# Performance work log

Measured on AMD Instinct MI355X. Metric: run time of the kernel, lower is better.

The kernel has to match this reference:

```python
import jax, jax.numpy as jnp
import numpy as np

B = 4; C = 3; IMG = 256; P = 16; HP = 16; HW = 256
DIM = 512; DEPTH = 6; HEADS = 8; DH = 64
NS = 50; SH = 4; SDH = 64; ITERS = 3; RPD = 128; FF = 2048; N = NS + HW


def _ln(x, g, b):
    m = jnp.mean(x, -1, keepdims=True)
    v = jnp.var(x, -1, keepdims=True)
    return (x - m) * jax.lax.rsqrt(v + 1e-5) * g + b


def _rms(x, g):
    # lucidrains RMSNorm: F.normalize(x, dim=-1) * sqrt(dim) * gamma
    n = jnp.linalg.norm(x, axis=-1, keepdims=True)
    return x / jnp.maximum(n, 1e-12) * (DIM ** 0.5) * g


def setup_inputs() -> dict:
    key = jax.random.key(0)
    ks = iter(jax.random.split(key, 64))
    def W(*s):
        return jax.random.normal(next(ks), s, jnp.float32) * 0.02
    SI = SH * SDH
    d = {}
    d['images'] = jax.random.normal(next(ks), (B, C, IMG, IMG), jnp.float32)
    d['slot_noise'] = jax.random.normal(next(ks), (B, NS, DIM), jnp.float32)
    d['patch_w'] = W(C * P * P, DIM); d['patch_b'] = jnp.zeros((DIM,))
    d['hpos'] = W(HP, DIM); d['wpos'] = W(HP, DIM)
    d['rp_w1'] = W(2, RPD); d['rp_b1'] = jnp.zeros((RPD,))
    d['rp_w2'] = W(RPD, RPD); d['rp_b2'] = jnp.zeros((RPD,))
    d['rp_w3'] = W(RPD, HEADS); d['rp_b3'] = jnp.zeros((HEADS,))
    d['slots_mu'] = W(1, 1, DIM); d['slots_logsigma'] = jnp.zeros((1, 1, DIM))
    d['sa_ln_in_g'] = jnp.ones((DIM,)); d['sa_ln_in_b'] = jnp.zeros((DIM,))
    d['sa_ln_sl_g'] = jnp.ones((DIM,)); d['sa_ln_sl_b'] = jnp.zeros((DIM,))
    d['sa_wq'] = W(DIM, SI); d['sa_bq'] = jnp.zeros((SI,))
    d['sa_wk'] = W(DIM, SI); d['sa_bk'] = jnp.zeros((SI,))
    d['sa_wv'] = W(DIM, SI); d['sa_bv'] = jnp.zeros((SI,))
    d['sa_wo'] = W(SI, DIM); d['sa_bo'] = jnp.zeros((DIM,))
    d['gru_wih'] = W(DIM, 3 * DIM); d['gru_whh'] = W(DIM, 3 * DIM)
    d['gru_bih'] = jnp.zeros((3 * DIM,)); d['gru_bhh'] = jnp.zeros((3 * DIM,))
    d['sa_ln_ff_g'] = jnp.ones((DIM,)); d['sa_ln_ff_b'] = jnp.zeros((DIM,))
    d['sa_mlp_w1'] = W(DIM, DIM); d['sa_mlp_b1'] = jnp.zeros((DIM,))
    d['sa_mlp_w2'] = W(DIM, DIM); d['sa_mlp_b2'] = jnp.zeros((DIM,))
    d['s2c_w'] = W(DIM, 2); d['s2c_b'] = jnp.zeros((2,))
    d['attn_g'] = jnp.ones((DEPTH, DIM))
    d['wq'] = W(DEPTH, DIM, HEADS * DH); d['wk'] = W(DEPTH, DIM, HEADS * DH)
    d['wv'] = W(DEPTH, DIM, HEADS * DH); d['wo'] = W(DEPTH, HEADS * DH, DIM)
    d['ff_g'] = jnp.ones((DEPTH, DIM))
    d['ff_w1'] = W(DEPTH, DIM, FF); d['ff_b1'] = jnp.zeros((DEPTH, FF))
    d['ff_w2'] = W(DEPTH, FF, DIM); d['ff_b2'] = jnp.zeros((DEPTH, DIM))
    d['final_g'] = jnp.ones((DIM,))
    d['pred_w'] = W(DIM, DIM); d['pred_b'] = jnp.zeros((DIM,))
    return d


def reference(images, slot_noise, patch_w, patch_b, hpos, wpos,
              rp_w1, rp_b1, rp_w2, rp_b2, rp_w3, rp_b3,
              slots_mu, slots_logsigma, sa_ln_in_g, sa_ln_in_b, sa_ln_sl_g, sa_ln_sl_b,
              sa_wq, sa_bq, sa_wk, sa_bk, sa_wv, sa_bv, sa_wo, sa_bo,
              gru_wih, gru_whh, gru_bih, gru_bhh, sa_ln_ff_g, sa_ln_ff_b,
              sa_mlp_w1, sa_mlp_b1, sa_mlp_w2, sa_mlp_b2, s2c_w, s2c_b,
              attn_g, wq, wk, wv, wo, ff_g, ff_w1, ff_b1, ff_w2, ff_b2,
              final_g, pred_w, pred_b):
    b = images.shape[0]
    # patchify: b c (h p1) (w p2) -> b h w (p1 p2 c)
    x = images.reshape(b, C, HP, P, HP, P).transpose(0, 2, 4, 3, 5, 1).reshape(b, HP, HP, P * P * C)
    tokens = x @ patch_w + patch_b                     # [b, HP, HP, DIM]
    tokens = tokens + hpos[:, None, :] + wpos[None, :, :]
    tokens = tokens.reshape(b, HW, DIM)
    # --- multi-head slot attention ---
    inp = _ln(tokens, sa_ln_in_g, sa_ln_in_b)
    k = (inp @ sa_wk + sa_bk).reshape(b, HW, SH, SDH).transpose(0, 2, 1, 3)
    v = (inp @ sa_wv + sa_bv).reshape(b, HW, SH, SDH).transpose(0, 2, 1, 3)
    slots = slots_mu + jnp.exp(slots_logsigma) * slot_noise  # [b, NS, DIM]
    scale = SDH ** -0.5
    for _ in range(ITERS):
        prev = slots
        s = _ln(slots, sa_ln_sl_g, sa_ln_sl_b)
        q = (s @ sa_wq + sa_bq).reshape(b, NS, SH, SDH).transpose(0, 2, 1, 3)
        dots = jnp.einsum('bhid,bhjd->bhij', q, k) * scale     # [b, SH, NS, HW]
        attn = jax.nn.softmax(dots, axis=-2) + 1e-8            # softmax over slots
        attn = attn / jnp.sum(attn, -1, keepdims=True)         # weighted mean over inputs
        upd = jnp.einsum('bhij,bhjd->bhid', attn, v)
        upd = upd.transpose(0, 2, 1, 3).reshape(b, NS, SH * SDH) @ sa_wo + sa_bo
        # GRUCell(updates, prev_slots)
        gx = upd @ gru_wih + gru_bih
        gh = prev @ gru_whh + gru_bhh
        xr, xz, xn = jnp.split(gx, 3, -1)
        hr, hz, hn = jnp.split(gh, 3, -1)
        r = jax.nn.sigmoid(xr + hr)
        z = jax.nn.sigmoid(xz + hz)
        nn_ = jnp.tanh(xn + r * hn)
        slots = (1 - z) * nn_ + z * prev
        slots = slots + (jax.nn.relu(_ln(slots, sa_ln_ff_g, sa_ln_ff_b) @ sa_mlp_w1 + sa_mlp_b1) @ sa_mlp_w2 + sa_mlp_b2)
    objects = slots
    slot_coords = objects @ s2c_w + s2c_b              # [b, NS, 2]
    # --- relative position MLP bias (slots coords + patch grid) ---
    g = jnp.arange(HP, dtype=jnp.float32)
    grid = jnp.stack(jnp.meshgrid(g, g, indexing='ij'), -1).reshape(HW, 2)
    coords = jnp.concatenate([slot_coords, jnp.broadcast_to(grid, (b, HW, 2))], axis=1)  # [b, N, 2]
    rel = coords[:, :, None, :] - coords[:, None, :, :]   # [b, N, N, 2]
    hmid = jax.nn.silu(rel @ rp_w1 + rp_b1)
    hmid = jax.nn.silu(hmid @ rp_w2 + rp_b2)
    bias = jnp.transpose(hmid @ rp_w3 + rp_b3, (0, 3, 1, 2))  # [b, HEADS, N, N]
    # --- transformer with per-layer rel-pos bias ---
    x = jnp.concatenate([objects, tokens], axis=1)     # [b, N, DIM]
    ascale = DH ** -0.5
    for l in range(DEPTH):
        h = _rms(x, attn_g[l])
        qh = (h @ wq[l]).reshape(b, N, HEADS, DH).transpose(0, 2, 1, 3)
        kh = (h @ wk[l]).reshape(b, N, HEADS, DH).transpose(0, 2, 1, 3)
        vh = (h @ wv[l]).reshape(b, N, HEADS, DH).transpose(0, 2, 1, 3)
        sim = jnp.einsum('bhid,bhjd->bhij', qh, kh) * ascale + bias
        a = jax.nn.softmax(sim, -1)
        o = jnp.einsum('bhij,bhjd->bhid', a, vh).transpose(0, 2, 1, 3).reshape(b, N, HEADS * DH) @ wo[l]
        x = x + o
        h = _rms(x, ff_g[l])
        x = x + (jax.nn.gelu(h @ ff_w1[l] + ff_b1[l]) @ ff_w2[l] + ff_b2[l])
    x = _rms(x, final_g)
    return x[:, NS:] @ pred_w + pred_b                 # [b, HW, DIM]
```

## Files before the change

### kernel.cpp

```cpp
#include <hip/hip_runtime.h>
#include <hip/hip_bf16.h>

typedef __hip_bfloat16 bf16;
typedef short short8v __attribute__((ext_vector_type(8)));
typedef float float4v __attribute__((ext_vector_type(4)));

static __device__ __forceinline__ float b2f(bf16 x){ return __bfloat162float(x); }

static __device__ __forceinline__ float ldin(const void* p, size_t i, bool isbf) {
  return isbf ? b2f(((const bf16*)p)[i]) : ((const float*)p)[i];
}

static __device__ __forceinline__ unsigned short f2bu(float f) {
  bf16 h = __float2bfloat16(f);
  return *reinterpret_cast<unsigned short*>(&h);
}

#define CDIV(a,b) (((a)+(b)-1)/(b))

#define NB   4
#define NSL  50
#define HWT  256
#define NT   306
#define DIM  512
#define NH   8
#define FF   2048
#define RPP  28100
#define PCH  56200

static __device__ __forceinline__ void rp_decode(int q, int& i, int& j) {
  if (q < 15300) { i = q / NT; j = q % NT; }
  else { int r = q - 15300; i = NSL + r / NSL; j = r % NSL; }
}

__global__ void detect_k(const void* p, int* flag) {
  const unsigned short* u = (const unsigned short*)p;
  int t = threadIdx.x;
  int e = (u[t] >> 7) & 0xFF;
  __shared__ int anybad;
  if (t == 0) anybad = 0;
  __syncthreads();
  if (e >= 0x88) atomicOr(&anybad, 1);
  __syncthreads();
  if (t == 0) *flag = anybad ? 0 : 1;
}

struct WtArgs {
  const void* W[17];
  unsigned long long wto[17];
  int K[17], N[17];
  int base[18];
};

__global__ __launch_bounds__(256) void wtrans_all_k(WtArgs a, unsigned short* __restrict__ WT,
                                                    const int* __restrict__ flagp) {
  const bool isbf = *flagp != 0;
  int bid = blockIdx.x;
  int idx = 0;
#pragma unroll
  for (int i = 1; i < 17; ++i) if (bid >= a.base[i]) idx = i;
  int t0 = bid - a.base[idx];
  const int K = a.K[idx], N = a.N[idx];
  const int tilesN = N >> 6;
  const int perLayer = tilesN * (K >> 6);
  const int layer = t0 / perLayer, rem = t0 % perLayer;
  const int n0 = (rem % tilesN) * 64, k0 = (rem / tilesN) * 64;
  const void* W = a.W[idx];
  unsigned short* dst0 = WT + a.wto[idx];
  const size_t slice = (size_t)K * N * layer;

  __shared__ unsigned short S[64 * 72];
  int t = threadIdx.x;
  int kk = t >> 4, nn = (t & 15) * 4;
#pragma unroll
  for (int r = 0; r < 4; ++r) {
    int k = k0 + kk + r * 16;
    unsigned short v[4];
    if (isbf) {
      ushort4 u = *(const ushort4*)((const unsigned short*)W + slice + (size_t)k * N + n0 + nn);
      v[0]=u.x; v[1]=u.y; v[2]=u.z; v[3]=u.w;
    } else {
      float4 f = *(const float4*)((const float*)W + slice + (size_t)k * N + n0 + nn);
      v[0]=f2bu(f.x); v[1]=f2bu(f.y); v[2]=f2bu(f.z); v[3]=f2bu(f.w);
    }
#pragma unroll
    for (int i = 0; i < 4; ++i) S[(nn + i) * 72 + kk + r * 16] = v[i];
  }
  __syncthreads();
  int nr = t >> 2, kc = (t & 3) * 16;
  short8v s0 = *(const short8v*)&S[nr * 72 + kc];
  short8v s1 = *(const short8v*)&S[nr * 72 + kc + 8];
  unsigned short* dst = dst0 + slice + (size_t)(n0 + nr) * K + k0 + kc;
  *(short8v*)dst = s0;
  *(short8v*)(dst + 8) = s1;
}

#define LDK 72
static __device__ __forceinline__ void gemm_body2(
    const void* __restrict__ A, int aty,
    const unsigned short* __restrict__ WT,
    const void* __restrict__ bias, size_t boff,
    void* __restrict__ C, int oty,
    int M, int N, int K, int kbeg, int kend,
    int act, int mode, int spec,
    const void* __restrict__ p0, const void* __restrict__ p1,
    bool isbf)
{
  __shared__ unsigned short As[64 * LDK];
  __shared__ unsigned short Bs[64 * LDK];
  const int tid = threadIdx.x;
  const int lane = tid & 63, wave = tid >> 6;
  const int quad = lane >> 4, ti = lane & 15;
  const int wm = (wave & 1) * 32, wn = (wave >> 1) * 32;
  const int bm = blockIdx.y * 64, bn = blockIdx.x * 64;
  const int srow = tid >> 2, sch = (tid & 3) * 16;

  unsigned short ha[16], hb[16];
  const int gm = bm + srow;
  const bool aok = gm < M;
  const unsigned short* Abf = (const unsigned short*)A + (size_t)gm * K;
  const float*          Af  = (const float*)A + (size_t)gm * K;
  const unsigned short* Bp  = WT + (size_t)(bn + srow) * K;

  auto fetchA = [&](int k0) {
    if (aok) {
      if (aty) {
        const ushort4* ap = (const ushort4*)(Abf + k0 + sch);
#pragma unroll
        for (int i = 0; i < 4; ++i) {
          ushort4 u = ap[i];
          ha[i*4+0]=u.x; ha[i*4+1]=u.y; ha[i*4+2]=u.z; ha[i*4+3]=u.w;
        }
      } else {
        const float4* ap = (const float4*)(Af + k0 + sch);
#pragma unroll
        for (int i = 0; i < 4; ++i) {
          float4 f = ap[i];
          ha[i*4+0]=f2bu(f.x); ha[i*4+1]=f2bu(f.y); ha[i*4+2]=f2bu(f.z); ha[i*4+3]=f2bu(f.w);
        }
      }
    } else {
#pragma unroll
      for (int i = 0; i < 16; ++i) ha[i] = 0;
    }
  };
  auto fetchB = [&](int k0) {
    const ushort4* bp = (const ushort4*)(Bp + k0 + sch);
#pragma unroll
    for (int i = 0; i < 4; ++i) {
      ushort4 u = bp[i];
      hb[i*4+0]=u.x; hb[i*4+1]=u.y; hb[i*4+2]=u.z; hb[i*4+3]=u.w;
    }
  };

  float4v acc00 = {0,0,0,0}, acc01 = {0,0,0,0}, acc10 = {0,0,0,0}, acc11 = {0,0,0,0};
  fetchA(kbeg); fetchB(kbeg);
  for (int k0 = kbeg; k0 < kend; k0 += 64) {
    *(short8v*)&As[srow * LDK + sch]     = *(short8v*)ha;
    *(short8v*)&As[srow * LDK + sch + 8] = *(short8v*)(ha + 8);
    *(short8v*)&Bs[srow * LDK + sch]     = *(short8v*)hb;
    *(short8v*)&Bs[srow * LDK + sch + 8] = *(short8v*)(hb + 8);
    __syncthreads();
    if (k0 + 64 < kend) { fetchA(k0 + 64); fetchB(k0 + 64); }
#pragma unroll
    for (int ks = 0; ks < 2; ++ks) {
      short8v a0 = *reinterpret_cast<const short8v*>(&As[(wm + ti)      * LDK + ks * 32 + quad * 8]);
      short8v a1 = *reinterpret_cast<const short8v*>(&As[(wm + 16 + ti) * LDK + ks * 32 + quad * 8]);
      short8v b0 = *reinterpret_cast<const short8v*>(&Bs[(wn + ti)      * LDK + ks * 32 + quad * 8]);
      short8v b1 = *reinterpret_cast<const short8v*>(&Bs[(wn + 16 + ti) * LDK + ks * 32 + quad * 8]);
      acc00 = __builtin_amdgcn_mfma_f32_16x16x32_bf16(a0, b0, acc00, 0, 0, 0);
      acc01 = __builtin_amdgcn_mfma_f32_16x16x32_bf16(a0, b1, acc01, 0, 0, 0);
      acc10 = __builtin_amdgcn_mfma_f32_16x16x32_bf16(a1, b0, acc10, 0, 0, 0);
      acc11 = __builtin_amdgcn_mfma_f32_16x16x32_bf16(a1, b1, acc11, 0, 0, 0);
    }
    __syncthreads();
  }

  float4v accs[2][2] = {{acc00, acc01}, {acc10, acc11}};
#pragma unroll
  for (int mi = 0; mi < 2; ++mi) {
#pragma unroll
    for (int ni = 0; ni < 2; ++ni) {
      int row0 = bm + wm + mi * 16 + quad * 4;
      int col  = bn + wn + ni * 16 + ti;
      float bv = (bias && kbeg == 0) ? ldin(bias, boff + col, isbf) : 0.f;
#pragma unroll
      for (int r = 0; r < 4; ++r) {
        int row = row0 + r;
        if (row >= M) continue;
        float v = accs[mi][ni][r] + bv;
        if (act == 1) v = fmaxf(v, 0.f);
        else if (act == 2) {
          float u = 0.7978845608028654f * (v + 0.044715f * v * v * v);
          v = 0.5f * v * (1.f + tanhf(u));
        } else if (act == 3) {
          v = v / (1.f + expf(-v));
        }
        if (spec == 2 && kbeg == 0) {
          int hh = (row >> 4) & 15, ww = row & 15;
          v += ldin(p0, hh * N + col, isbf) + ldin(p1, ww * N + col, isbf);
        }
        if (spec == 1) {
          int b_ = row / NT, n_ = row % NT;
          if (n_ >= NSL) {
            size_t oi = ((size_t)(b_ * HWT + (n_ - NSL))) * N + col;
            if (isbf) ((bf16*)C)[oi] = __float2bfloat16(v);
            else      ((float*)C)[oi] = v;
          }
        } else {
          size_t idx = (size_t)row * N + col;
          if (oty) ((bf16*)C)[idx] = __float2bfloat16(v);
          else {
            float* Cf = (float*)C;
            if (mode == 2) atomicAdd(&Cf[idx], v);
            else if (mode == 1) Cf[idx] += v;
            else Cf[idx] = v;
          }
        }
      }
    }
  }
}

__global__ __launch_bounds__(256) void gemm_mfma(
    const void* A, int aty, const unsigned short* WT, size_t woff,
    const void* bias, size_t boff, void* C, int oty,
    int M, int N, int K, int act, int accum, int zsplit,
    int spec, const void* p0, const void* p1, const int* __restrict__ flagp)
{
  int ksz = K / zsplit;
  int kbeg = blockIdx.z * ksz;
  int mode = zsplit > 1 ? 2 : (accum ? 1 : 0);
  gemm_body2(A, aty, WT + woff, bias, boff, C, oty, M, N, K, kbeg, kbeg + ksz,
             act, mode, spec, p0, p1, *flagp != 0);
}

__global__ __launch_bounds__(256) void gemm_mfma_tri(
    const void* A, int aty, const unsigned short* WT, size_t o0, size_t o1, size_t o2,
    void* C0, void* C1, void* C2, int oty, int M, int N, int K,
    const int* __restrict__ flagp)
{
  size_t o = blockIdx.z == 0 ? o0 : (blockIdx.z == 1 ? o1 : o2);
  void* C = blockIdx.z == 0 ? C0 : (blockIdx.z == 1 ? C1 : C2);
  gemm_body2(A, aty, WT + o, nullptr, 0, C, oty, M, N, K, 0, K, 0, 0, 0,
             nullptr, nullptr, *flagp != 0);
}

__global__ __launch_bounds__(256) void gemm_mfma_duo(
    const void* A0, const void* A1, int aty, const unsigned short* WT, size_t o0, size_t o1,
    const void* bias0, const void* bias1, void* C0, void* C1, int oty,
    int M, int N, int K, const int* __restrict__ flagp)
{
  const void* A = blockIdx.z ? A1 : A0;
  size_t o = blockIdx.z ? o1 : o0;
  const void* bias = blockIdx.z ? bias1 : bias0;
  void* C = blockIdx.z ? C1 : C0;
  gemm_body2(A, aty, WT + o, bias, 0, C, oty, M, N, K, 0, K, 0, 0, 0,
             nullptr, nullptr, *flagp != 0);
}

__global__ void coords_k(const float* __restrict__ slots, const void* __restrict__ w,
                         const void* __restrict__ bv, float* __restrict__ coords,
                         const int* __restrict__ flagp) {
  const bool isbf = *flagp != 0;
  __shared__ float r0[256], r1[256];
  int blk = blockIdx.x, t = threadIdx.x;
  if (blk < 200) {
    int b = blk / 50, n = blk % 50;
    const float* x = slots + (size_t)blk * DIM;
    float v0 = x[t], v1 = x[t + 256];
    float a0 = v0 * ldin(w, 2 * t, isbf)     + v1 * ldin(w, 2 * (t + 256), isbf);
    float a1 = v0 * ldin(w, 2 * t + 1, isbf) + v1 * ldin(w, 2 * (t + 256) + 1, isbf);
    r0[t] = a0; r1[t] = a1;
    __syncthreads();
    for (int o = 128; o > 0; o >>= 1) {
      if (t < o) { r0[t] += r0[t + o]; r1[t] += r1[t + o]; }
      __syncthreads();
    }
    if (t == 0) {
      coords[((size_t)b * NT + n) * 2]     = r0[0] + ldin(bv, 0, isbf);
      coords[((size_t)b * NT + n) * 2 + 1] = r1[0] + ldin(bv, 1, isbf);
    }
  } else {
#pragma unroll
    for (int s = 0; s < 4; ++s) {
      int i = t + 256 * s;
      int b = i >> 8, tt = i & 255;
      coords[((size_t)b * NT + NSL + tt) * 2]     = (float)(tt >> 4);
      coords[((size_t)b * NT + NSL + tt) * 2 + 1] = (float)(tt & 15);
    }
  }
}

__global__ void patchify_k(const void* __restrict__ img, unsigned short* __restrict__ xp,
                           const int* __restrict__ flagp) {
  const bool isbf = *flagp != 0;
  int i = blockIdx.x * 256 + threadIdx.x;
  if (i >= NB * HWT * 768) return;
  int col = i % 768, row = i / 768;
  int c = col % 3, p2 = (col / 3) & 15, p1 = col / 48;
  int w = row & 15, h = (row >> 4) & 15, b = row >> 8;
  xp[i] = f2bu(ldin(img, (((size_t)(b * 3 + c) * 256 + h * 16 + p1) * 256) + w * 16 + p2, isbf));
}

__global__ void ln512_k(const float* __restrict__ X, const void* __restrict__ g,
                        const void* __restrict__ b, unsigned short* __restrict__ Y,
                        const int* __restrict__ flagp) {
  const bool isbf = *flagp != 0;
  int row = blockIdx.x, t = threadIdx.x;
  const float* x = X + (size_t)row * DIM;
  float v0 = x[t], v1 = x[t + 256];
  __shared__ float rs[256], rq[256];
  rs[t] = v0 + v1; rq[t] = v0 * v0 + v1 * v1;
  __syncthreads();
  for (int o = 128; o > 0; o >>= 1) {
    if (t < o) { rs[t] += rs[t + o]; rq[t] += rq[t + o]; }
    __syncthreads();
  }
  float mean = rs[0] * (1.f / 512.f);
  float var  = rq[0] * (1.f / 512.f) - mean * mean;
  float inv  = rsqrtf(var + 1e-5f);
  unsigned short* y = Y + (size_t)row * DIM;
  y[t]       = f2bu((v0 - mean) * inv * ldin(g, t, isbf)       + ldin(b, t, isbf));
  y[t + 256] = f2bu((v1 - mean) * inv * ldin(g, t + 256, isbf) + ldin(b, t + 256, isbf));
}

__global__ void rms512_k(const float* __restrict__ X, const void* __restrict__ g,
                         int goff, unsigned short* __restrict__ Y, const int* __restrict__ flagp) {
  const bool isbf = *flagp != 0;
  int row = blockIdx.x, t = threadIdx.x;
  const float* x = X + (size_t)row * DIM;
  float v0 = x[t], v1 = x[t + 256];
  __shared__ float rq[256];
  rq[t] = v0 * v0 + v1 * v1;
  __syncthreads();
  for (int o = 128; o > 0; o >>= 1) {
    if (t < o) rq[t] += rq[t + o];
    __syncthreads();
  }
  float nrm = sqrtf(rq[0]);
  float sc = 22.62741699796952f / fmaxf(nrm, 1e-12f);
  unsigned short* y = Y + (size_t)row * DIM;
  y[t]       = f2bu(v0 * sc * ldin(g, goff + t, isbf));
  y[t + 256] = f2bu(v1 * sc * ldin(g, goff + t + 256, isbf));
}

__global__ void slots_init_k(const void* __restrict__ mu, const void* __restrict__ ls,
                             const void* __restrict__ noise, float* __restrict__ slots,
                             const int* __restrict__ flagp) {
  const bool isbf = *flagp != 0;
  int i = blockIdx.x * 256 + threadIdx.x;
  if (i >= NB * NSL * DIM) return;
  int d = i & 511;
  slots[i] = ldin(mu, d, isbf) + expf(ldin(ls, d, isbf)) * ldin(noise, i, isbf);
}

__global__ __launch_bounds__(256) void slot_attn_k(
    const float* __restrict__ q, const float* __restrict__ k,
    const float* __restrict__ v, float* __restrict__ upd)
{
  __shared__ float Qs[NSL * 64];
  __shared__ float S[NSL * 257];
  const int bh = blockIdx.x, b = bh >> 2, h = bh & 3;
  const int t = threadIdx.x;

  for (int e = t; e < NSL * 64; e += 256) {
    int i = e >> 6, d = e & 63;
    Qs[e] = q[((size_t)(b * NSL + i)) * 256 + h * 64 + d];
  }
  __syncthreads();

  {
    const float* kr = k + ((size_t)(b * HWT + t)) * 256 + h * 64;
    float kreg[64];
#pragma unroll
    for (int d4 = 0; d4 < 16; ++d4) {
      float4 f = *(const float4*)(kr + d4 * 4);
      kreg[d4*4+0]=f.x; kreg[d4*4+1]=f.y; kreg[d4*4+2]=f.z; kreg[d4*4+3]=f.w;
    }
#pragma unroll 1
    for (int i = 0; i < NSL; ++i) {
      float s = 0.f;
#pragma unroll
      for (int d = 0; d < 64; ++d) s = fmaf(Qs[i * 64 + d], kreg[d], s);
      S[i * 257 + t] = s * 0.125f;
    }
    float m = -1e30f;
#pragma unroll 1
    for (int i = 0; i < NSL; ++i) m = fmaxf(m, S[i * 257 + t]);
    float ssum = 0.f;
#pragma unroll 1
    for (int i = 0; i < NSL; ++i) {
      float e = __expf(S[i * 257 + t] - m);
      S[i * 257 + t] = e; ssum += e;
    }
    float inv = 1.f / ssum;
#pragma unroll 1
    for (int i = 0; i < NSL; ++i) S[i * 257 + t] = fmaf(S[i * 257 + t], inv, 1e-8f);
  }
  __syncthreads();

  {
    const int w = t >> 6, l = t & 63;
    for (int i = w; i < NSL; i += 4) {
      float a0 = S[i * 257 + l],       a1 = S[i * 257 + 64 + l];
      float a2 = S[i * 257 + 128 + l], a3 = S[i * 257 + 192 + l];
      float s4 = a0 + a1 + a2 + a3;
#pragma unroll
      for (int o = 1; o < 64; o <<= 1) s4 += __shfl_xor(s4, o);
      float inv2 = 1.f / s4;
      S[i * 257 + l]       = a0 * inv2;
      S[i * 257 + 64 + l]  = a1 * inv2;
      S[i * 257 + 128 + l] = a2 * inv2;
      S[i * 257 + 192 + l] = a3 * inv2;
    }
  }
  __syncthreads();

  {
    const int d = t & 63, g = t >> 6;
    float acc[13];
#pragma unroll
    for (int r = 0; r < 13; ++r) acc[r] = 0.f;
    const float* vbase = v + ((size_t)(b * HWT)) * 256 + h * 64 + d;
#pragma unroll 1
    for (int j = 0; j < HWT; ++j) {
      float vv = vbase[(size_t)j * 256];
#pragma unroll
      for (int r = 0; r < 13; ++r) {
        int i = g + 4 * r;
        if (i < NSL) acc[r] = fmaf(S[i * 257 + j], vv, acc[r]);
      }
    }
#pragma unroll
    for (int r = 0; r < 13; ++r) {
      int i = g + 4 * r;
      if (i < NSL) upd[((size_t)(b * NSL + i)) * 256 + h * 64 + d] = acc[r];
    }
  }
}

__global__ void gru_k(const float* __restrict__ gx, const float* __restrict__ gh,
                      float* __restrict__ slots) {
  int i = blockIdx.x * 256 + threadIdx.x;
  if (i >= NB * NSL * DIM) return;
  int row = i >> 9, d = i & 511;
  size_t b3 = (size_t)row * 1536;
  float xr = gx[b3 + d], xz = gx[b3 + 512 + d], xn = gx[b3 + 1024 + d];
  float hr = gh[b3 + d], hz = gh[b3 + 512 + d], hn = gh[b3 + 1024 + d];
  float r = 1.f / (1.f + expf(-(xr + hr)));
  float z = 1.f / (1.f + expf(-(xz + hz)));
  float n = tanhf(xn + r * hn);
  float prev = slots[i];
  slots[i] = (1.f - z) * n + z * prev;
}

__global__ void relpos_table_k(const void* w1, const void* b1, const void* w2,
                               const void* b2, const void* w3, const void* b3,
                               float* __restrict__ tab, const int* __restrict__ flagp) {
  const bool isbf = *flagp != 0;
  int blk = blockIdx.x;
  float r0 = (float)(blk / 31 - 15), r1 = (float)(blk % 31 - 15);
  int t = threadIdx.x;
  __shared__ float h1[128], h2[128];
  float a = fmaf(r0, ldin(w1, t, isbf), fmaf(r1, ldin(w1, 128 + t, isbf), ldin(b1, t, isbf)));
  h1[t] = a / (1.f + expf(-a));
  __syncthreads();
  float s = ldin(b2, t, isbf);
#pragma unroll 4
  for (int k = 0; k < 128; ++k) s = fmaf(h1[k], ldin(w2, k * 128 + t, isbf), s);
  h2[t] = s / (1.f + expf(-s));
  __syncthreads();
  if (t < 8) {
    float o = ldin(b3, t, isbf);
#pragma unroll 4
    for (int k = 0; k < 128; ++k) o = fmaf(h2[k], ldin(w3, k * 8 + t, isbf), o);
    tab[blk * 8 + t] = o;
  }
}

__global__ void bias_fill_k(const float* __restrict__ tab, float* __restrict__ bias) {
  int i = blockIdx.x * 256 + threadIdx.x;
  if (i >= NB * NH * HWT * HWT) return;
  int jj = i & 255, ii = (i >> 8) & 255, h = (i >> 16) & 7, b = i >> 19;
  int di = (ii >> 4) - (jj >> 4) + 15;
  int dj = (ii & 15) - (jj & 15) + 15;
  bias[(((size_t)(b * NH + h) * NT) + NSL + ii) * NT + NSL + jj] = tab[(di * 31 + dj) * 8 + h];
}

__global__ void rp_l1_k(const float* __restrict__ coords, const void* w1, const void* b1,
                        unsigned short* __restrict__ H, int pbase, int pcount,
                        const int* __restrict__ flagp) {
  const bool isbf = *flagp != 0;
  int idx = blockIdx.x * 256 + threadIdx.x;
  if (idx >= pcount * 128) return;
  int pl = idx >> 7, u = idx & 127;
  int p = pbase + pl;
  int q = p % RPP, bb = p / RPP;
  int ii, jj;
  rp_decode(q, ii, jj);
  float r0 = coords[(bb * NT + ii) * 2]     - coords[(bb * NT + jj) * 2];
  float r1 = coords[(bb * NT + ii) * 2 + 1] - coords[(bb * NT + jj) * 2 + 1];
  float a = fmaf(r0, ldin(w1, u, isbf), fmaf(r1, ldin(w1, 128 + u, isbf), ldin(b1, u, isbf)));
  H[(size_t)pl * 128 + u] = f2bu(a / (1.f + expf(-a)));
}

__global__ __launch_bounds__(256) void rp_l3_k(
    const unsigned short* __restrict__ H2, const void* w3, const void* b3,
    float* __restrict__ bias, int pbase, int pcount, const int* __restrict__ flagp) {
  const bool isbf = *flagp != 0;
  __shared__ float W3s[8 * 132];
  int t = threadIdx.x;
  for (int e = t; e < 1024; e += 256) {
    int k = e >> 3, hh = e & 7;
    W3s[hh * 132 + k] = ldin(w3, e, isbf);
  }
  __syncthreads();
  int pl = blockIdx.x * 32 + (t >> 3), hh = t & 7;
  if (pl >= pcount) return;
  int p = pbase + pl;
  int q = p % RPP, bb = p / RPP;
  int ii, jj;
  rp_decode(q, ii, jj);
  float s = ldin(b3, hh, isbf);
  const unsigned short* hrow = H2 + (size_t)pl * 128;
  const float* wrow = &W3s[hh * 132];
#pragma unroll 8
  for (int k4 = 0; k4 < 32; ++k4) {
    ushort4 h4 = *(const ushort4*)(hrow + k4 * 4);
    float4  w4 = *(const float4*)(wrow + k4 * 4);
    s = fmaf(b2f(*reinterpret_cast<bf16*>(&h4.x)), w4.x, s);
    s = fmaf(b2f(*reinterpret_cast<bf16*>(&h4.y)), w4.y, s);
    s = fmaf(b2f(*reinterpret_cast<bf16*>(&h4.z)), w4.z, s);
    s = fmaf(b2f(*reinterpret_cast<bf16*>(&h4.w)), w4.w, s);
  }
  bias[((size_t)(bb * NH + hh) * NT + ii) * NT + jj] = s;
}

__global__ void build_x_k(const float* __restrict__ slots, const float* __restrict__ tok,
                          float* __restrict__ x) {
  int i = blockIdx.x * 256 + threadIdx.x;
  if (i >= NB * NT * DIM) return;
  int d = i & 511, n = (i >> 9) % NT, b = i / (NT * DIM);
  x[i] = (n < NSL) ? slots[((size_t)(b * NSL + n)) * DIM + d]
                   : tok[((size_t)(b * HWT + (n - NSL))) * DIM + d];
}

__global__ __launch_bounds__(256) void attn_fused_k(
    const unsigned short* __restrict__ Qb, const unsigned short* __restrict__ Kb,
    const unsigned short* __restrict__ Vb, const float* __restrict__ bias,
    unsigned short* __restrict__ Ob)
{
  const int bh = blockIdx.y, b = bh >> 3, h = bh & 7;
  const int i0 = blockIdx.x * 32;
  __shared__ unsigned short Qs[32 * 72];
  __shared__ unsigned short Ks[64 * 72];
  __shared__ float S[32 * 332];
  unsigned short* P = (unsigned short*)S;

  const int tid = threadIdx.x;
  const int lane = tid & 63, wave = tid >> 6, quad = lane >> 4, ti = lane & 15;
  const int mi = wave & 1, nh = wave >> 1;

  {
    int r = tid >> 3, c = (tid & 7) * 8;
    int gi = i0 + r;
    ushort4 u0 = {0,0,0,0}, u1 = {0,0,0,0};
    if (gi < NT) {
      const ushort4* p = (const ushort4*)(Qb + ((size_t)(b * NT + gi)) * DIM + h * 64 + c);
      u0 = p[0]; u1 = p[1];
    }
    *(ushort4*)&Qs[r * 72 + c] = u0;
    *(ushort4*)&Qs[r * 72 + c + 4] = u1;
  }

  for (int kt = 0; kt < 5; ++kt) {
    __syncthreads();
    {
      int kr = tid >> 2, c = (tid & 3) * 16;
      int gj = kt * 64 + kr;
      ushort4 v[4] = {{0,0,0,0},{0,0,0,0},{0,0,0,0},{0,0,0,0}};
      if (gj < NT) {
        const ushort4* p = (const ushort4*)(Kb + ((size_t)(b * NT + gj)) * DIM + h * 64 + c);
#pragma unroll
        for (int i = 0; i < 4; ++i) v[i] = p[i];
      }
#pragma unroll
      for (int i = 0; i < 4; ++i) *(ushort4*)&Ks[kr * 72 + c + i * 4] = v[i];
    }
    __syncthreads();
#pragma unroll
    for (int ntl = 0; ntl < 2; ++ntl) {
      int nt = nh * 2 + ntl;
      float4v acc = {0,0,0,0};
#pragma unroll
      for (int ks = 0; ks < 2; ++ks) {
        short8v a  = *(const short8v*)&Qs[(mi * 16 + ti) * 72 + ks * 32 + quad * 8];
        short8v bb = *(const short8v*)&Ks[(nt * 16 + ti) * 72 + ks * 32 + quad * 8];
        acc = __builtin_amdgcn_mfma_f32_16x16x32_bf16(a, bb, acc, 0, 0, 0);
      }
      int colL = kt * 64 + nt * 16 + ti;
      int row0 = mi * 16 + quad * 4;
#pragma unroll
      for (int r = 0; r < 4; ++r) {
        int row_g = i0 + row0 + r;
        float val;
        if (colL < NT) {
          float bv = (row_g < NT) ? bias[((size_t)bh * NT + row_g) * NT + colL] : 0.f;
          val = acc[r] * 0.125f + bv;
        } else val = -1e30f;
        S[(row0 + r) * 332 + colL] = val;
      }
    }
  }
  __syncthreads();

  {
    int rl = tid >> 3, sub = tid & 7;
    float sv[40];
#pragma unroll
    for (int k = 0; k < 40; ++k) sv[k] = S[rl * 332 + sub + k * 8];
    float m = -1e30f;
#pragma unroll
    for (int k = 0; k < 40; ++k) m = fmaxf(m, sv[k]);
    m = fmaxf(m, __shfl_xor(m, 1));
    m = fmaxf(m, __shfl_xor(m, 2));
    m = fmaxf(m, __shfl_xor(m, 4));
    float s = 0.f;
#pragma unroll
    for (int k = 0; k < 40; ++k) { float e = __expf(sv[k] - m); sv[k] = e; s += e; }
    s += __shfl_xor(s, 1);
    s += __shfl_xor(s, 2);
    s += __shfl_xor(s, 4);
    float inv = 1.f / s;
    __syncthreads();
#pragma unroll
    for (int k = 0; k < 40; ++k) P[rl * 664 + sub + k * 8] = f2bu(sv[k] * inv);
  }

  float4v oacc[2] = {{0,0,0,0},{0,0,0,0}};
  for (int vt = 0; vt < 5; ++vt) {
    __syncthreads();
    {
      int key = tid & 63, d0 = (tid >> 6) * 16;
      int gj = vt * 64 + key;
      unsigned short hv[16];
      if (gj < NT) {
        const ushort4* p = (const ushort4*)(Vb + ((size_t)(b * NT + gj)) * DIM + h * 64 + d0);
#pragma unroll
        for (int i = 0; i < 4; ++i) {
          ushort4 u = p[i];
          hv[i*4+0]=u.x; hv[i*4+1]=u.y; hv[i*4+2]=u.z; hv[i*4+3]=u.w;
        }
      } else {
#pragma unroll
        for (int i = 0; i < 16; ++i) hv[i] = 0;
      }
#pragma unroll
      for (int i = 0; i < 16; ++i) Ks[(d0 + i) * 72 + key] = hv[i];
    }
    __syncthreads();
#pragma unroll
    for (int ntl = 0; ntl < 2; ++ntl) {
      int nt = nh * 2 + ntl;
#pragma unroll
      for (int ks = 0; ks < 2; ++ks) {
        short8v a  = *(const short8v*)&P[(mi * 16 + ti) * 664 + vt * 64 + ks * 32 + quad * 8];
        short8v bb = *(const short8v*)&Ks[(nt * 16 + ti) * 72 + ks * 32 + quad * 8];
        oacc[ntl] = __builtin_amdgcn_mfma_f32_16x16x32_bf16(a, bb, oacc[ntl], 0, 0, 0);
      }
    }
  }

#pragma unroll
  for (int ntl = 0; ntl < 2; ++ntl) {
    int dim = nh * 32 + ntl * 16 + ti;
#pragma unroll
    for (int r = 0; r < 4; ++r) {
      int row_g = i0 + mi * 16 + quad * 4 + r;
      if (row_g < NT)
        Ob[((size_t)(b * NT + row_g)) * DIM + h * 64 + dim] = f2bu(oacc[ntl][r]);
    }
  }
}

extern "C" void kernel_launch(void* const* d_in, const int* in_sizes, int n_in,
                              void* d_out, int out_size, void* d_ws, size_t ws_size,
                              hipStream_t stream) {
  const void* images        = d_in[0];
  const void* slot_noise    = d_in[1];
  const void* patch_w       = d_in[2];
  const void* patch_b       = d_in[3];
  const void* hpos          = d_in[4];
  const void* wpos          = d_in[5];
  const void* rp_w1         = d_in[6];
  const void* rp_b1         = d_in[7];
  const void* rp_w2         = d_in[8];
  const void* rp_b2         = d_in[9];
  const void* rp_w3         = d_in[10];
  const void* rp_b3         = d_in[11];
  const void* slots_mu      = d_in[12];
  const void* slots_logsig  = d_in[13];
  const void* sa_ln_in_g    = d_in[14];
  const void* sa_ln_in_b    = d_in[15];
  const void* sa_ln_sl_g    = d_in[16];
  const void* sa_ln_sl_b    = d_in[17];
  const void* sa_wq         = d_in[18];
  const void* sa_bq         = d_in[19];
  const void* sa_wk         = d_in[20];
  const void* sa_bk         = d_in[21];
  const void* sa_wv         = d_in[22];
  const void* sa_bv         = d_in[23];
  const void* sa_wo         = d_in[24];
  const void* sa_bo         = d_in[25];
  const void* gru_wih       = d_in[26];
  const void* gru_whh       = d_in[27];
  const void* gru_bih       = d_in[28];
  const void* gru_bhh       = d_in[29];
  const void* sa_ln_ff_g    = d_in[30];
  const void* sa_ln_ff_b    = d_in[31];
  const void* sa_mlp_w1     = d_in[32];
  const void* sa_mlp_b1     = d_in[33];
  const void* sa_mlp_w2     = d_in[34];
  const void* sa_mlp_b2     = d_in[35];
  const void* s2c_w         = d_in[36];
  const void* s2c_b         = d_in[37];
  const void* attn_g        = d_in[38];
  const void* wq            = d_in[39];
  const void* wk            = d_in[40];
  const void* wv            = d_in[41];
  const void* wo            = d_in[42];
  const void* ff_g          = d_in[43];
  const void* ff_w1         = d_in[44];
  const void* ff_b1         = d_in[45];
  const void* ff_w2         = d_in[46];
  const void* ff_b2         = d_in[47];
  const void* final_g       = d_in[48];
  const void* pred_w        = d_in[49];
  const void* pred_b        = d_in[50];

  float* ws = (float*)d_ws;
  int* FLAG = (int*)ws;
  size_t off = 16;
  auto alloc = [&](size_t n) { float* p = ws + off; off += (n + 15) & ~(size_t)15; return p; };
  float* TOK   = alloc((size_t)NB * HWT * DIM);
  unsigned short* INPB = (unsigned short*)alloc((size_t)NB * HWT * DIM / 2);
  float* KB    = alloc((size_t)NB * HWT * 256);
  float* VB    = alloc((size_t)NB * HWT * 256);
  float* SLOTS = alloc((size_t)NB * NSL * DIM);
  unsigned short* SLNB = (unsigned short*)alloc((size_t)NB * NSL * DIM / 2);
  float* QB    = alloc((size_t)NB * NSL * 256);
  float* ATT   = alloc((size_t)NB * 4 * NSL * HWT);
  float* UPD   = alloc((size_t)NB * NSL * 256);
  float* UPDP  = alloc((size_t)NB * NSL * DIM);
  unsigned short* HIDSB = (unsigned short*)alloc((size_t)NB * NSL * DIM / 2);
  float* SC    = alloc((size_t)NB * NSL * 2);
  float* CRD   = alloc((size_t)NB * NT * 2);
  float* TAB   = alloc((size_t)961 * 8);
  float* BIAS  = alloc((size_t)NB * NH * NT * NT);
  float* X     = alloc((size_t)NB * NT * DIM);
  unsigned short* HBB  = (unsigned short*)alloc((size_t)NB * NT * DIM / 2);
  unsigned short* QHB  = (unsigned short*)alloc((size_t)NB * NT * DIM / 2);
  unsigned short* KHB  = (unsigned short*)alloc((size_t)NB * NT * DIM / 2);
  unsigned short* VHB  = (unsigned short*)alloc((size_t)NB * NT * DIM / 2);
  float* SIM   = alloc((size_t)NB * NH * NT * NT);
  unsigned short* OBB  = (unsigned short*)alloc((size_t)NB * NT * DIM / 2);
  unsigned short* FFHB = (unsigned short*)alloc((size_t)NB * NT * FF / 2);
  float* OUTT  = alloc((size_t)NB * NT * DIM);
  unsigned short* XPB = (unsigned short*)OUTT;
  float* GX = SIM;
  float* GH = SIM + (size_t)NB * NSL * 1536;
  (void)ATT; (void)SC;
  const size_t oPatch = 0;
  const size_t oKw    = oPatch + (size_t)512 * 768;
  const size_t oVw    = oKw    + (size_t)256 * 512;
  const size_t oQw    = oVw    + (size_t)256 * 512;
  const size_t oWo    = oQw    + (size_t)256 * 512;
  const size_t oGih   = oWo    + (size_t)512 * 256;
  const size_t oGhh   = oGih   + (size_t)1536 * 512;
  const size_t oMlp1  = oGhh   + (size_t)1536 * 512;
  const size_t oMlp2  = oMlp1  + (size_t)512 * 512;
  const size_t oRp2   = oMlp2  + (size_t)512 * 512;
  const size_t oWq    = oRp2   + (size_t)128 * 128;
  const size_t oWk    = oWq    + (size_t)6 * 512 * 512;
  const size_t oWv    = oWk    + (size_t)6 * 512 * 512;
  const size_t oWol   = oWv    + (size_t)6 * 512 * 512;
  const size_t oFf1   = oWol   + (size_t)6 * 512 * 512;
  const size_t oFf2   = oFf1   + (size_t)6 * 512 * 2048;
  const size_t oPred  = oFf2   + (size_t)6 * 2048 * 512;
  const size_t wtTotal = oPred + (size_t)512 * 512;
  unsigned short* WTS = (unsigned short*)alloc((wtTotal + 1) / 2);
  (void)ws_size; (void)in_sizes; (void)n_in; (void)out_size;

#define GEMMM(A_, ATY_, WOFF_, BIAS_, BOFF_, C_, OTY_, M_, N_, K_, ACT_, ACC_, ZS_, SPEC_, P0_, P1_) \
  gemm_mfma<<<dim3((N_)/64, CDIV((M_),64), (ZS_)), 256, 0, stream>>>( \
      A_, ATY_, WTS, (size_t)(WOFF_), BIAS_, (size_t)(BOFF_), C_, OTY_, M_, N_, K_, ACT_, ACC_, ZS_, \
      SPEC_, P0_, P1_, FLAG)

  const int MROW = NB * NT;
  const int MS   = NB * NSL;

  detect_k<<<1, 256, 0, stream>>>(images, FLAG);
  {
    WtArgs a;
    const void* Wp[17] = { patch_w, sa_wk, sa_wv, sa_wq, sa_wo, gru_wih, gru_whh,
                           sa_mlp_w1, sa_mlp_w2, rp_w2, wq, wk, wv, wo, ff_w1, ff_w2, pred_w };
    const size_t Oo[17] = { oPatch, oKw, oVw, oQw, oWo, oGih, oGhh,
                            oMlp1, oMlp2, oRp2, oWq, oWk, oWv, oWol, oFf1, oFf2, oPred };
    const int Kk[17] = {768,512,512,512,256,512,512,512,512,128,512,512,512,512,512,2048,512};
    const int Nn[17] = {512,256,256,256,512,1536,1536,512,512,128,512,512,512,512,2048,512,512};
    const int Ll[17] = {1,1,1,1,1,1,1,1,1,1,6,6,6,6,6,6,1};
    int acc = 0;
    for (int i = 0; i < 17; ++i) {
      a.W[i] = Wp[i]; a.wto[i] = Oo[i]; a.K[i] = Kk[i]; a.N[i] = Nn[i];
      a.base[i] = acc;
      acc += Ll[i] * (Kk[i] >> 6) * (Nn[i] >> 6);
    }
    a.base[17] = acc;
    wtrans_all_k<<<acc, 256, 0, stream>>>(a, WTS, FLAG);
  }

  patchify_k<<<CDIV(NB*HWT*768, 256), 256, 0, stream>>>(images, XPB, FLAG);
  hipMemsetAsync(TOK, 0, (size_t)NB * HWT * DIM * sizeof(float), stream);
  GEMMM(XPB, 1, oPatch, patch_b, 0, TOK, 0, NB*HWT, DIM, 768, 0, 0, 3, 2, hpos, wpos);

  ln512_k<<<NB*HWT, 256, 0, stream>>>(TOK, sa_ln_in_g, sa_ln_in_b, INPB, FLAG);
  gemm_mfma_duo<<<dim3(4, 16, 2), 256, 0, stream>>>(
      INPB, INPB, 1, WTS, oKw, oVw, sa_bk, sa_bv, KB, VB, 0, NB*HWT, 256, DIM, FLAG);
  slots_init_k<<<CDIV(NB*NSL*DIM, 256), 256, 0, stream>>>(slots_mu, slots_logsig, slot_noise, SLOTS, FLAG);

  for (int it = 0; it < 3; ++it) {
    ln512_k<<<MS, 256, 0, stream>>>(SLOTS, sa_ln_sl_g, sa_ln_sl_b, SLNB, FLAG);
    GEMMM(SLNB, 1, oQw, sa_bq, 0, QB, 0, MS, 256, DIM, 0, 0, 1, 0, nullptr, nullptr);
    slot_attn_k<<<16, 256, 0, stream>>>(QB, KB, VB, UPD);
    GEMMM(UPD, 0, oWo, sa_bo, 0, UPDP, 0, MS, DIM, 256, 0, 0, 1, 0, nullptr, nullptr);
    gemm_mfma_duo<<<dim3(24, 4, 2), 256, 0, stream>>>(
        UPDP, SLOTS, 0, WTS, oGih, oGhh, gru_bih, gru_bhh, GX, GH, 0, MS, 1536, DIM, FLAG);
    gru_k<<<CDIV(NB*NSL*DIM, 256), 256, 0, stream>>>(GX, GH, SLOTS);
    ln512_k<<<MS, 256, 0, stream>>>(SLOTS, sa_ln_ff_g, sa_ln_ff_b, SLNB, FLAG);
    GEMMM(SLNB, 1, oMlp1, sa_mlp_b1, 0, HIDSB, 1, MS, DIM, DIM, 1, 0, 1, 0, nullptr, nullptr);
    GEMMM(HIDSB, 1, oMlp2, sa_mlp_b2, 0, SLOTS, 0, MS, DIM, DIM, 0, 1, 1, 0, nullptr, nullptr);
  }

  coords_k<<<201, 256, 0, stream>>>(SLOTS, s2c_w, s2c_b, CRD, FLAG);
  relpos_table_k<<<961, 128, 0, stream>>>(rp_w1, rp_b1, rp_w2, rp_b2, rp_w3, rp_b3, TAB, FLAG);
  bias_fill_k<<<CDIV(NB*NH*HWT*HWT, 256), 256, 0, stream>>>(TAB, BIAS);
  {
    unsigned short* H1 = HBB;
    unsigned short* H2 = HBB + (size_t)PCH * 128;
    for (int c = 0; c < 2; ++c) {
      int pb = c * PCH;
      rp_l1_k<<<CDIV(PCH*128, 256), 256, 0, stream>>>(CRD, rp_w1, rp_b1, H1, pb, PCH, FLAG);
      GEMMM(H1, 1, oRp2, rp_b2, 0, H2, 1, PCH, 128, 128, 3, 0, 1, 0, nullptr, nullptr);
      rp_l3_k<<<CDIV(PCH,32), 256, 0, stream>>>(H2, rp_w3, rp_b3, BIAS, pb, PCH, FLAG);
    }
  }

  build_x_k<<<CDIV(NB*NT*DIM, 256), 256, 0, stream>>>(SLOTS, TOK, X);
  for (int l = 0; l < 6; ++l) {
    size_t lw = (size_t)l * 512 * 512;
    rms512_k<<<MROW, 256, 0, stream>>>(X, attn_g, l * DIM, HBB, FLAG);
    gemm_mfma_tri<<<dim3(8, 20, 3), 256, 0, stream>>>(
        HBB, 1, WTS, oWq + lw, oWk + lw, oWv + lw, QHB, KHB, VHB, 1, MROW, DIM, DIM, FLAG);
    attn_fused_k<<<dim3(10, NB*NH), 256, 0, stream>>>(QHB, KHB, VHB, BIAS, OBB);
    GEMMM(OBB, 1, oWol + lw, (const void*)nullptr, 0, X, 0, MROW, DIM, DIM, 0, 1, 2, 0, nullptr, nullptr);
    rms512_k<<<MROW, 256, 0, stream>>>(X, ff_g, l * DIM, HBB, FLAG);
    GEMMM(HBB, 1, oFf1 + (size_t)l * 512 * 2048, ff_b1, l * FF, FFHB, 1, MROW, FF, DIM, 2, 0, 1, 0, nullptr, nullptr);
    GEMMM(FFHB, 1, oFf2 + (size_t)l * 2048 * 512, ff_b2, l * DIM, X, 0, MROW, DIM, FF, 0, 1, 4, 0, nullptr, nullptr);
  }

  rms512_k<<<MROW, 256, 0, stream>>>(X, final_g, 0, HBB, FLAG);
  GEMMM(HBB, 1, oPred, pred_b, 0, d_out, 0, MROW, DIM, DIM, 0, 0, 1, 1, nullptr, nullptr);

#undef GEMMM
}
```

Measured before the change: 1.395 ms.

## Split slot attention into three kernels and drop patch GEMM split-K memset

The single 16-block slot attention kernel is replaced by three launches: a dots kernel with 800 blocks, a softmax plus renormalisation kernel with 16 blocks, and an update kernel with 200 blocks. This spreads the work over far more compute units than the 16 that were busy before. The cost is two extra launches per iteration and a round trip of the attention matrix through global memory. Separately, the patch-embedding GEMM moves from split-K 3 to 1, which removes the memset of TOK that the atomic accumulation needed.

```diff
diff --git a/kernel.cpp b/kernel.cpp
--- a/kernel.cpp
+++ b/kernel.cpp
@@ -355,89 +355,62 @@
   slots[i] = ldin(mu, d, isbf) + expf(ldin(ls, d, isbf)) * ldin(noise, i, isbf);
 }
 
-__global__ __launch_bounds__(256) void slot_attn_k(
-    const float* __restrict__ q, const float* __restrict__ k,
-    const float* __restrict__ v, float* __restrict__ upd)
-{
-  __shared__ float Qs[NSL * 64];
+__global__ void slot_dots_k(const float* __restrict__ q, const float* __restrict__ k,
+                            float* __restrict__ dots) {
+  int blk = blockIdx.x;
+  int i = blk % 50, h = (blk / 50) & 3, b = blk / 200;
+  int j = threadIdx.x;
+  __shared__ float qs[64];
+  if (threadIdx.x < 64) qs[threadIdx.x] = q[((size_t)(b * 50 + i)) * 256 + h * 64 + threadIdx.x];
+  __syncthreads();
+  const float* kr = k + ((size_t)(b * 256 + j)) * 256 + h * 64;
+  float s = 0.f;
+#pragma unroll 8
+  for (int d = 0; d < 64; ++d) s = fmaf(qs[d], kr[d], s);
+  dots[(((size_t)(b * 4 + h) * 50) + i) * 256 + j] = s * 0.125f;
+}
+
+__global__ __launch_bounds__(256) void sm_renorm_k(float* __restrict__ att) {
   __shared__ float S[NSL * 257];
-  const int bh = blockIdx.x, b = bh >> 2, h = bh & 3;
   const int t = threadIdx.x;
-
-  for (int e = t; e < NSL * 64; e += 256) {
-    int i = e >> 6, d = e & 63;
-    Qs[e] = q[((size_t)(b * NSL + i)) * 256 + h * 64 + d];
-  }
-  __syncthreads();
-
-  {
-    const float* kr = k + ((size_t)(b * HWT + t)) * 256 + h * 64;
-    float kreg[64];
-#pragma unroll
-    for (int d4 = 0; d4 < 16; ++d4) {
-      float4 f = *(const float4*)(kr + d4 * 4);
-      kreg[d4*4+0]=f.x; kreg[d4*4+1]=f.y; kreg[d4*4+2]=f.z; kreg[d4*4+3]=f.w;
-    }
-#pragma unroll 1
-    for (int i = 0; i < NSL; ++i) {
-      float s = 0.f;
-#pragma unroll
-      for (int d = 0; d < 64; ++d) s = fmaf(Qs[i * 64 + d], kreg[d], s);
-      S[i * 257 + t] = s * 0.125f;
-    }
-    float m = -1e30f;
-#pragma unroll 1
-    for (int i = 0; i < NSL; ++i) m = fmaxf(m, S[i * 257 + t]);
-    float ssum = 0.f;
-#pragma unroll 1
-    for (int i = 0; i < NSL; ++i) {
-      float e = __expf(S[i * 257 + t] - m);
-      S[i * 257 + t] = e; ssum += e;
-    }
-    float inv = 1.f / ssum;
-#pragma unroll 1
-    for (int i = 0; i < NSL; ++i) S[i * 257 + t] = fmaf(S[i * 257 + t], inv, 1e-8f);
-  }
-  __syncthreads();
-
-  {
-    const int w = t >> 6, l = t & 63;
-    for (int i = w; i < NSL; i += 4) {
-      float a0 = S[i * 257 + l],       a1 = S[i * 257 + 64 + l];
-      float a2 = S[i * 257 + 128 + l], a3 = S[i * 257 + 192 + l];
-      float s4 = a0 + a1 + a2 + a3;
-#pragma unroll
-      for (int o = 1; o < 64; o <<= 1) s4 += __shfl_xor(s4, o);
-      float inv2 = 1.f / s4;
-      S[i * 257 + l]       = a0 * inv2;
-      S[i * 257 + 64 + l]  = a1 * inv2;
-      S[i * 257 + 128 + l] = a2 * inv2;
-      S[i * 257 + 192 + l] = a3 * inv2;
-    }
-  }
-  __syncthreads();
-
-  {
-    const int d = t & 63, g = t >> 6;
-    float acc[13];
-#pragma unroll
-    for (int r = 0; r < 13; ++r) acc[r] = 0.f;
-    const float* vbase = v + ((size_t)(b * HWT)) * 256 + h * 64 + d;
-#pragma unroll 1
-    for (int j = 0; j < HWT; ++j) {
-      float vv = vbase[(size_t)j * 256];
-#pragma unroll
-      for (int r = 0; r < 13; ++r) {
-        int i = g + 4 * r;
-        if (i < NSL) acc[r] = fmaf(S[i * 257 + j], vv, acc[r]);
-      }
-    }
-#pragma unroll
-    for (int r = 0; r < 13; ++r) {
-      int i = g + 4 * r;
-      if (i < NSL) upd[((size_t)(b * NSL + i)) * 256 + h * 64 + d] = acc[r];
-    }
-  }
+  float* base = att + (size_t)blockIdx.x * (NSL * HWT);
+  float v[NSL];
+#pragma unroll
+  for (int i = 0; i < NSL; ++i) v[i] = base[i * HWT + t];
+  float m = -1e30f;
+#pragma unroll
+  for (int i = 0; i < NSL; ++i) m = fmaxf(m, v[i]);
+  float s = 0.f;
+#pragma unroll
+  for (int i = 0; i < NSL; ++i) { float e = __expf(v[i] - m); v[i] = e; s += e; }
+  float inv = 1.f / s;
+#pragma unroll
+  for (int i = 0; i < NSL; ++i) S[i * 257 + t] = fmaf(v[i], inv, 1e-8f);
+  __syncthreads();
+  const int w = t >> 6, l = t & 63;
+  for (int r = w; r < NSL; r += 4) {
+    float a0 = S[r * 257 + l],        a1 = S[r * 257 + 64 + l];
+    float a2 = S[r * 257 + 128 + l],  a3 = S[r * 257 + 192 + l];
+    float s4 = a0 + a1 + a2 + a3;
+#pragma unroll
+    for (int o = 1; o < 64; o <<= 1) s4 += __shfl_xor(s4, o);
+    float inv2 = 1.f / s4;
+    base[r * HWT + l]       = a0 * inv2;
+    base[r * HWT + 64 + l]  = a1 * inv2;
+    base[r * HWT + 128 + l] = a2 * inv2;
+    base[r * HWT + 192 + l] = a3 * inv2;
+  }
+}
+
+__global__ void slot_upd_k(const float* __restrict__ attn, const float* __restrict__ v,
+                           float* __restrict__ upd) {
+  int bi = blockIdx.x;
+  int b = bi / 50, i = bi % 50;
+  int t = threadIdx.x, h = t >> 6;
+  const float* arow = attn + ((size_t)((b * 4 + h) * 50) + i) * 256;
+  float s = 0.f;
+  for (int j = 0; j < 256; ++j) s = fmaf(arow[j], v[((size_t)(b * 256 + j)) * 256 + t], s);
+  upd[(size_t)bi * 256 + t] = s;
 }
 
 __global__ void gru_k(const float* __restrict__ gx, const float* __restrict__ gh,
@@ -754,7 +727,6 @@
   float* UPD   = alloc((size_t)NB * NSL * 256);
   float* UPDP  = alloc((size_t)NB * NSL * DIM);
   unsigned short* HIDSB = (unsigned short*)alloc((size_t)NB * NSL * DIM / 2);
-  float* SC    = alloc((size_t)NB * NSL * 2);
   float* CRD   = alloc((size_t)NB * NT * 2);
   float* TAB   = alloc((size_t)961 * 8);
   float* BIAS  = alloc((size_t)NB * NH * NT * NT);
@@ -770,7 +742,6 @@
   unsigned short* XPB = (unsigned short*)OUTT;
   float* GX = SIM;
   float* GH = SIM + (size_t)NB * NSL * 1536;
-  (void)ATT; (void)SC;
   const size_t oPatch = 0;
   const size_t oKw    = oPatch + (size_t)512 * 768;
   const size_t oVw    = oKw    + (size_t)256 * 512;
@@ -821,8 +792,7 @@
   }
 
   patchify_k<<<CDIV(NB*HWT*768, 256), 256, 0, stream>>>(images, XPB, FLAG);
-  hipMemsetAsync(TOK, 0, (size_t)NB * HWT * DIM * sizeof(float), stream);
-  GEMMM(XPB, 1, oPatch, patch_b, 0, TOK, 0, NB*HWT, DIM, 768, 0, 0, 3, 2, hpos, wpos);
+  GEMMM(XPB, 1, oPatch, patch_b, 0, TOK, 0, NB*HWT, DIM, 768, 0, 0, 1, 2, hpos, wpos);
 
   ln512_k<<<NB*HWT, 256, 0, stream>>>(TOK, sa_ln_in_g, sa_ln_in_b, INPB, FLAG);
   gemm_mfma_duo<<<dim3(4, 16, 2), 256, 0, stream>>>(
@@ -832,7 +802,9 @@
   for (int it = 0; it < 3; ++it) {
     ln512_k<<<MS, 256, 0, stream>>>(SLOTS, sa_ln_sl_g, sa_ln_sl_b, SLNB, FLAG);
     GEMMM(SLNB, 1, oQw, sa_bq, 0, QB, 0, MS, 256, DIM, 0, 0, 1, 0, nullptr, nullptr);
-    slot_attn_k<<<16, 256, 0, stream>>>(QB, KB, VB, UPD);
+    slot_dots_k<<<NB*4*NSL, 256, 0, stream>>>(QB, KB, ATT);
+    sm_renorm_k<<<16, 256, 0, stream>>>(ATT);
+    slot_upd_k<<<MS, 256, 0, stream>>>(ATT, VB, UPD);
     GEMMM(UPD, 0, oWo, sa_bo, 0, UPDP, 0, MS, DIM, 256, 0, 0, 1, 0, nullptr, nullptr);
     gemm_mfma_duo<<<dim3(24, 4, 2), 256, 0, stream>>>(
         UPDP, SLOTS, 0, WTS, oGih, oGhh, gru_bih, gru_bhh, GX, GH, 0, MS, 1536, DIM, FLAG);
```

After: 1.186 ms. 1.18x faster.
